# Kernel optimization log

Measured on AMD Instinct MI355X. Metric: run time of the kernel, lower is better.

## Reference

```python
import jax, jax.numpy as jnp
import numpy as np

B, T, I, H, G = 4096, 1024, 1, 16, 48  # G = 3*H gates

def _gru_layer(inp, w_ih, w_hh, b_ih, b_hh):
    # inp: [B, T, Din] -> out: [B, T, H]. PyTorch GRU gate math.
    # Precompute all input-side gate projections once (batched GEMM).
    xg = jnp.einsum('btd,gd->tbg', inp, w_ih) + b_ih  # [T, B, 3H]

    def step(h, xg_t):
        hg = h @ w_hh.T + b_hh                         # [B, 3H]
        xr, xz, xn = jnp.split(xg_t, 3, axis=-1)
        hr, hz, hn = jnp.split(hg, 3, axis=-1)
        r = jax.nn.sigmoid(xr + hr)
        z = jax.nn.sigmoid(xz + hz)
        n = jnp.tanh(xn + r * hn)
        h_new = (1.0 - z) * n + z * h
        return h_new, h_new

    h0 = jnp.zeros((inp.shape[0], H), dtype=inp.dtype)
    _, ys = jax.lax.scan(step, h0, xg)                 # ys: [T, B, H]
    return jnp.transpose(ys, (1, 0, 2))                # [B, T, H]

def setup_inputs() -> dict:
    key = jax.random.key(0)
    ks = jax.random.split(key, 8)
    s = 1.0 / np.sqrt(H)  # PyTorch default uniform(-1/sqrt(H), 1/sqrt(H))
    u = lambda k, shape: jax.random.uniform(k, shape, jnp.float32, -s, s)
    return {
        'x':      jax.random.normal(ks[0], (B, T, I), jnp.float32),
        'w_ih0':  u(ks[1], (G, I)),
        'w_ih12': u(ks[2], (2, G, H)),
        'w_hh':   u(ks[3], (3, G, H)),
        'b_ih':   u(ks[4], (3, G)),
        'b_hh':   u(ks[5], (3, G)),
        'fc_w':   u(ks[6], (5, H)),
        'fc_b':   u(ks[7], (5,)),
    }

def reference(x, w_ih0, w_ih12, w_hh, b_ih, b_hh, fc_w, fc_b):
    # 3-layer GRU (dropout=0.3 between layers is identity in eval mode)
    h = _gru_layer(x, w_ih0,     w_hh[0], b_ih[0], b_hh[0])
    h = _gru_layer(h, w_ih12[0], w_hh[1], b_ih[1], b_hh[1])
    h = _gru_layer(h, w_ih12[1], w_hh[2], b_ih[2], b_hh[2])
    # Linear head on the last timestep
    return h[:, -1, :] @ fc_w.T + fc_b                 # [B, 5]
```

## Files before the change

kernel.cpp:

```cpp
#include <hip/hip_runtime.h>
#include <stdint.h>

#define TSTEPS 1024
#define L2E 1.4426950408889634f
#define XPITCH 1028

typedef float v2f __attribute__((ext_vector_type(2)));
typedef float v4f __attribute__((ext_vector_type(4)));

__device__ __forceinline__ float rcpf_(float v) { return __builtin_amdgcn_rcpf(v); }
__device__ __forceinline__ float ex2(float v) { return __builtin_amdgcn_exp2f(v); }
#define PKFMA(a, b, c) __builtin_elementwise_fma((a), (b), (c))

__device__ __forceinline__ v2f ldg2(const float* p) {
    v2f r; uint64_t a = (uint64_t)p;
    asm volatile("global_load_dwordx2 %0, %1, off\n\ts_waitcnt vmcnt(0)"
                 : "=v"(r) : "v"(a));
    return r;
}
__device__ __forceinline__ float ldg1(const float* p) {
    float r; uint64_t a = (uint64_t)p;
    asm volatile("global_load_dword %0, %1, off\n\ts_waitcnt vmcnt(0)"
                 : "=v"(r) : "v"(a));
    return r;
}

#define RDH(dst, p)                                                        \
    do {                                                                   \
        v4f a0 = *(const v4f*)(p);                                         \
        v4f a1 = *(const v4f*)((p) + 4);                                   \
        v4f a2 = *(const v4f*)((p) + 8);                                   \
        v4f a3 = *(const v4f*)((p) + 12);                                  \
        dst[0] = __builtin_shufflevector(a0, a0, 0, 1);                    \
        dst[1] = __builtin_shufflevector(a0, a0, 2, 3);                    \
        dst[2] = __builtin_shufflevector(a1, a1, 0, 1);                    \
        dst[3] = __builtin_shufflevector(a1, a1, 2, 3);                    \
        dst[4] = __builtin_shufflevector(a2, a2, 0, 1);                    \
        dst[5] = __builtin_shufflevector(a2, a2, 2, 3);                    \
        dst[6] = __builtin_shufflevector(a3, a3, 0, 1);                    \
        dst[7] = __builtin_shufflevector(a3, a3, 2, 3);                    \
    } while (0)

#define DOT8(w, h, seed)                                                   \
    ({                                                                     \
        v2f _a = PKFMA(w[0], h[0], (seed));                                \
        _a = PKFMA(w[1], h[1], _a); _a = PKFMA(w[2], h[2], _a);            \
        _a = PKFMA(w[3], h[3], _a); _a = PKFMA(w[4], h[4], _a);            \
        _a = PKFMA(w[5], h[5], _a); _a = PKFMA(w[6], h[6], _a);            \
        _a = PKFMA(w[7], h[7], _a);                                        \
        _a.x + _a.y;                                                       \
    })
#define DOT16(wa, ha, wb, hb, seed)                                        \
    ({                                                                     \
        v2f _a = PKFMA(wa[0], ha[0], (seed));                              \
        _a = PKFMA(wa[1], ha[1], _a); _a = PKFMA(wa[2], ha[2], _a);        \
        _a = PKFMA(wa[3], ha[3], _a); _a = PKFMA(wa[4], ha[4], _a);        \
        _a = PKFMA(wa[5], ha[5], _a); _a = PKFMA(wa[6], ha[6], _a);        \
        _a = PKFMA(wa[7], ha[7], _a);                                      \
        _a = PKFMA(wb[0], hb[0], _a); _a = PKFMA(wb[1], hb[1], _a);        \
        _a = PKFMA(wb[2], hb[2], _a); _a = PKFMA(wb[3], hb[3], _a);        \
        _a = PKFMA(wb[4], hb[4], _a); _a = PKFMA(wb[5], hb[5], _a);        \
        _a = PKFMA(wb[6], hb[6], _a); _a = PKFMA(wb[7], hb[7], _a);        \
        _a.x + _a.y;                                                       \
    })

__global__ __launch_bounds__(768, 3)
__attribute__((amdgpu_waves_per_eu(3, 3)))
void gru3_ws(
    const float* __restrict__ x,
    const float* __restrict__ w_ih0,
    const float* __restrict__ w_ih12,
    const float* __restrict__ w_hh,
    const float* __restrict__ b_ih,
    const float* __restrict__ b_hh,
    const float* __restrict__ fc_w,
    const float* __restrict__ fc_b,
    float* __restrict__ out)
{
    __shared__ float xs[16 * XPITCH];
    __shared__ float hbuf[2][16][3][16];

    const int tid = threadIdx.x;
    const int wave = tid >> 6;
    const int role = wave >> 2;
    const int lane = tid & 63;
    const int s = lane >> 4;
    const int u = lane & 15;
    const int lseq = (wave & 3) * 4 + s;
    const int seq = blockIdx.x * 16 + lseq;

    {
        const float4* xg = (const float4*)(x + (size_t)blockIdx.x * 16 * TSTEPS);
#pragma unroll
        for (int j = 0; j < 6; ++j) {
            int idx = tid + 768 * j;
            if (idx < 4096) {
                float4 v = xg[idx];
                *(float4*)&xs[(idx >> 8) * XPITCH + (idx & 255) * 4] = v;
            }
        }
        ((float*)hbuf)[tid] = 0.f;
        if (tid < 1536 - 768) ((float*)hbuf)[768 + tid] = 0.f;
    }
    __syncthreads();

    if (role == 0) {
        v2f wr[8], wz[8], wn[8];
#pragma unroll
        for (int m = 0; m < 8; ++m) {
            wr[m] = ldg2(w_hh + (0 * 48 + u) * 16 + 2 * m) * -L2E;
            wz[m] = ldg2(w_hh + (0 * 48 + 16 + u) * 16 + 2 * m) * -L2E;
            wn[m] = ldg2(w_hh + (0 * 48 + 32 + u) * 16 + 2 * m) * (2.f * L2E);
        }
        const float wxr = ldg1(w_ih0 + u) * -L2E;
        const float wxz = ldg1(w_ih0 + 16 + u) * -L2E;
        const float wxn = ldg1(w_ih0 + 32 + u) * (2.f * L2E);
        const v2f sbr = {-(ldg1(b_ih + u) + ldg1(b_hh + u)) * L2E, 0.f};
        const v2f sbz = {-(ldg1(b_ih + 16 + u) + ldg1(b_hh + 16 + u)) * L2E, 0.f};
        const v2f sbn = {ldg1(b_hh + 32 + u) * (2.f * L2E), 0.f};
        const float bnx = ldg1(b_ih + 32 + u) * (2.f * L2E);
        const float* xrow = &xs[lseq * XPITCH];
        float* wb0 = &hbuf[0][lseq][0][0];
        float* wb1 = &hbuf[1][lseq][0][0];
        float hown = 0.f;
#pragma unroll 2
        for (int k = 0; k < 1026; ++k) {
            if (k < 1024) {
                const float* rb = (k & 1) ? wb0 : wb1;
                v2f hp[8];
                RDH(hp, rb);
                float xt = xrow[k];
                float sr = fmaf(wxr, xt, DOT8(wr, hp, sbr));
                float sz = fmaf(wxz, xt, DOT8(wz, hp, sbz));
                float snh = DOT8(wn, hp, sbn);
                float r = rcpf_(1.f + ex2(sr));
                float z = rcpf_(1.f + ex2(sz));
                float ut = fmaf(r, snh, fmaf(wxn, xt, bnx));
                float n = fmaf(-2.f, rcpf_(ex2(ut) + 1.f), 1.f);
                hown = fmaf(z, hown - n, n);
                ((k & 1) ? wb1 : wb0)[u] = hown;
            }
            __syncthreads();
        }
    } else if (role == 1) {
        v2f wr[8], wz[8], wn[8], vr[8], vz[8], vn[8];
#pragma unroll
        for (int m = 0; m < 8; ++m) {
            wr[m] = ldg2(w_hh + (48 + u) * 16 + 2 * m) * -L2E;
            wz[m] = ldg2(w_hh + (48 + 16 + u) * 16 + 2 * m) * -L2E;
            wn[m] = ldg2(w_hh + (48 + 32 + u) * 16 + 2 * m) * (2.f * L2E);
            vr[m] = ldg2(w_ih12 + (u) * 16 + 2 * m) * -L2E;
            vz[m] = ldg2(w_ih12 + (16 + u) * 16 + 2 * m) * -L2E;
            vn[m] = ldg2(w_ih12 + (32 + u) * 16 + 2 * m) * (2.f * L2E);
        }
        const v2f sbr = {-(ldg1(b_ih + 48 + u) + ldg1(b_hh + 48 + u)) * L2E, 0.f};
        const v2f sbz = {-(ldg1(b_ih + 64 + u) + ldg1(b_hh + 64 + u)) * L2E, 0.f};
        const v2f sbn = {ldg1(b_hh + 80 + u) * (2.f * L2E), 0.f};
        const v2f sbx = {ldg1(b_ih + 80 + u) * (2.f * L2E), 0.f};
        float* base0 = &hbuf[0][lseq][0][0];
        float* base1 = &hbuf[1][lseq][0][0];
        float hown = 0.f;
#pragma unroll 2
        for (int k = 0; k < 1026; ++k) {
            if (k >= 1 && k <= 1024) {
                const float* rb = (k & 1) ? base0 : base1;
                v2f hin[8], hp[8];
                RDH(hin, rb);
                RDH(hp, rb + 16);
                float sr = DOT16(wr, hp, vr, hin, sbr);
                float sz = DOT16(wz, hp, vz, hin, sbz);
                float snh = DOT8(wn, hp, sbn);
                float snx = DOT8(vn, hin, sbx);
                float r = rcpf_(1.f + ex2(sr));
                float z = rcpf_(1.f + ex2(sz));
                float ut = fmaf(r, snh, snx);
                float n = fmaf(-2.f, rcpf_(ex2(ut) + 1.f), 1.f);
                hown = fmaf(z, hown - n, n);
                ((k & 1) ? base1 : base0)[16 + u] = hown;
            }
            __syncthreads();
        }
    } else {
        v2f wr[8], wz[8], wn[8], vr[8], vz[8], vn[8];
#pragma unroll
        for (int m = 0; m < 8; ++m) {
            wr[m] = ldg2(w_hh + (96 + u) * 16 + 2 * m) * -L2E;
            wz[m] = ldg2(w_hh + (96 + 16 + u) * 16 + 2 * m) * -L2E;
            wn[m] = ldg2(w_hh + (96 + 32 + u) * 16 + 2 * m) * (2.f * L2E);
            vr[m] = ldg2(w_ih12 + (48 + u) * 16 + 2 * m) * -L2E;
            vz[m] = ldg2(w_ih12 + (48 + 16 + u) * 16 + 2 * m) * -L2E;
            vn[m] = ldg2(w_ih12 + (48 + 32 + u) * 16 + 2 * m) * (2.f * L2E);
        }
        const v2f sbr = {-(ldg1(b_ih + 96 + u) + ldg1(b_hh + 96 + u)) * L2E, 0.f};
        const v2f sbz = {-(ldg1(b_ih + 112 + u) + ldg1(b_hh + 112 + u)) * L2E, 0.f};
        const v2f sbn = {ldg1(b_hh + 128 + u) * (2.f * L2E), 0.f};
        const v2f sbx = {ldg1(b_ih + 128 + u) * (2.f * L2E), 0.f};
        float* base0 = &hbuf[0][lseq][0][0];
        float* base1 = &hbuf[1][lseq][0][0];
        float hown = 0.f;
#pragma unroll 2
        for (int k = 0; k < 1026; ++k) {
            if (k >= 2) {
                const float* rb = (k & 1) ? base0 : base1;
                v2f hin[8], hp[8];
                RDH(hin, rb + 16);
                RDH(hp, rb + 32);
                float sr = DOT16(wr, hp, vr, hin, sbr);
                float sz = DOT16(wz, hp, vz, hin, sbz);
                float snh = DOT8(wn, hp, sbn);
                float snx = DOT8(vn, hin, sbx);
                float r = rcpf_(1.f + ex2(sr));
                float z = rcpf_(1.f + ex2(sz));
                float ut = fmaf(r, snh, snx);
                float n = fmaf(-2.f, rcpf_(ex2(ut) + 1.f), 1.f);
                hown = fmaf(z, hown - n, n);
                ((k & 1) ? base1 : base0)[32 + u] = hown;
            }
            __syncthreads();
        }
        if (u < 5) {
            const float* h2f = &hbuf[1][lseq][2][0];
            float acc = fc_b[u];
#pragma unroll
            for (int j = 0; j < 16; ++j)
                acc = fmaf(fc_w[u * 16 + j], h2f[j], acc);
            out[seq * 5 + u] = acc;
        }
    }
}

extern "C" void kernel_launch(void* const* d_in, const int* in_sizes, int n_in,
                              void* d_out, int out_size, void* d_ws, size_t ws_size,
                              hipStream_t stream) {
    const float* x      = (const float*)d_in[0];
    const float* w_ih0  = (const float*)d_in[1];
    const float* w_ih12 = (const float*)d_in[2];
    const float* w_hh   = (const float*)d_in[3];
    const float* b_ih   = (const float*)d_in[4];
    const float* b_hh   = (const float*)d_in[5];
    const float* fc_w   = (const float*)d_in[6];
    const float* fc_b   = (const float*)d_in[7];
    float* out = (float*)d_out;

    gru3_ws<<<256, 768, 0, stream>>>(
        x, w_ih0, w_ih12, w_hh, b_ih, b_hh, fc_w, fc_b, out);
}
```

Before: 513.2 us.

## Batch four timesteps per barrier with per-layer ring buffers and smaller blocks

Measured after the change: 492.3 us. 4.1% less time.

```diff
diff --git a/kernel.cpp b/kernel.cpp
--- a/kernel.cpp
+++ b/kernel.cpp
@@ -2,6 +2,8 @@
 #include <stdint.h>
 
 #define TSTEPS 1024
+#define S 4
+#define NK 258
 #define L2E 1.4426950408889634f
 #define XPITCH 1028
 
@@ -64,9 +66,9 @@
         _a.x + _a.y;                                                       \
     })
 
-__global__ __launch_bounds__(768, 3)
+__global__ __launch_bounds__(192, 3)
 __attribute__((amdgpu_waves_per_eu(3, 3)))
-void gru3_ws(
+void gru3_sk(
     const float* __restrict__ x,
     const float* __restrict__ w_ih0,
     const float* __restrict__ w_ih12,
@@ -77,30 +79,30 @@
     const float* __restrict__ fc_b,
     float* __restrict__ out)
 {
-    __shared__ float xs[16 * XPITCH];
-    __shared__ float hbuf[2][16][3][16];
+    __shared__ float xs[4][XPITCH];
+    __shared__ float hring[3][2][S][4][16];
+    __shared__ float h2f[4][16];
 
     const int tid = threadIdx.x;
-    const int wave = tid >> 6;
-    const int role = wave >> 2;
+    const int role = tid >> 6;
     const int lane = tid & 63;
     const int s = lane >> 4;
     const int u = lane & 15;
-    const int lseq = (wave & 3) * 4 + s;
-    const int seq = blockIdx.x * 16 + lseq;
+    const int seq = blockIdx.x * 4 + s;
 
     {
-        const float4* xg = (const float4*)(x + (size_t)blockIdx.x * 16 * TSTEPS);
+        const float4* xg = (const float4*)(x + (size_t)blockIdx.x * 4 * TSTEPS);
 #pragma unroll
         for (int j = 0; j < 6; ++j) {
-            int idx = tid + 768 * j;
-            if (idx < 4096) {
+            int idx = tid + 192 * j;
+            if (idx < 1024) {
                 float4 v = xg[idx];
-                *(float4*)&xs[(idx >> 8) * XPITCH + (idx & 255) * 4] = v;
-            }
-        }
-        ((float*)hbuf)[tid] = 0.f;
-        if (tid < 1536 - 768) ((float*)hbuf)[768 + tid] = 0.f;
+                *(float4*)&xs[idx >> 8][(idx & 255) * 4] = v;
+            }
+        }
+#pragma unroll
+        for (int j = 0; j < 8; ++j)
+            ((float*)hring)[tid + 192 * j] = 0.f;
     }
     __syncthreads();
 
@@ -108,9 +110,9 @@
         v2f wr[8], wz[8], wn[8];
 #pragma unroll
         for (int m = 0; m < 8; ++m) {
-            wr[m] = ldg2(w_hh + (0 * 48 + u) * 16 + 2 * m) * -L2E;
-            wz[m] = ldg2(w_hh + (0 * 48 + 16 + u) * 16 + 2 * m) * -L2E;
-            wn[m] = ldg2(w_hh + (0 * 48 + 32 + u) * 16 + 2 * m) * (2.f * L2E);
+            wr[m] = ldg2(w_hh + (u) * 16 + 2 * m) * -L2E;
+            wz[m] = ldg2(w_hh + (16 + u) * 16 + 2 * m) * -L2E;
+            wn[m] = ldg2(w_hh + (32 + u) * 16 + 2 * m) * (2.f * L2E);
         }
         const float wxr = ldg1(w_ih0 + u) * -L2E;
         const float wxz = ldg1(w_ih0 + 16 + u) * -L2E;
@@ -119,28 +121,32 @@
         const v2f sbz = {-(ldg1(b_ih + 16 + u) + ldg1(b_hh + 16 + u)) * L2E, 0.f};
         const v2f sbn = {ldg1(b_hh + 32 + u) * (2.f * L2E), 0.f};
         const float bnx = ldg1(b_ih + 32 + u) * (2.f * L2E);
-        const float* xrow = &xs[lseq * XPITCH];
-        float* wb0 = &hbuf[0][lseq][0][0];
-        float* wb1 = &hbuf[1][lseq][0][0];
+        float* cur = &hring[0][0][0][s][0];
+        float* prv = &hring[0][1][0][s][0];
         float hown = 0.f;
-#pragma unroll 2
-        for (int k = 0; k < 1026; ++k) {
-            if (k < 1024) {
-                const float* rb = (k & 1) ? wb0 : wb1;
-                v2f hp[8];
-                RDH(hp, rb);
-                float xt = xrow[k];
-                float sr = fmaf(wxr, xt, DOT8(wr, hp, sbr));
-                float sz = fmaf(wxz, xt, DOT8(wz, hp, sbz));
-                float snh = DOT8(wn, hp, sbn);
-                float r = rcpf_(1.f + ex2(sr));
-                float z = rcpf_(1.f + ex2(sz));
-                float ut = fmaf(r, snh, fmaf(wxn, xt, bnx));
-                float n = fmaf(-2.f, rcpf_(ex2(ut) + 1.f), 1.f);
-                hown = fmaf(z, hown - n, n);
-                ((k & 1) ? wb1 : wb0)[u] = hown;
+        for (int K = 0; K < NK; ++K) {
+            if (K < 256) {
+                v4f xq = *(const v4f*)&xs[s][K * S];
+#pragma unroll
+                for (int j = 0; j < S; ++j) {
+                    const float* rb = (j == 0) ? (prv + (S - 1) * 64)
+                                               : (cur + (j - 1) * 64);
+                    v2f hp[8];
+                    RDH(hp, rb);
+                    float xt = xq[j];
+                    float sr = fmaf(wxr, xt, DOT8(wr, hp, sbr));
+                    float sz = fmaf(wxz, xt, DOT8(wz, hp, sbz));
+                    float snh = DOT8(wn, hp, sbn);
+                    float r = rcpf_(1.f + ex2(sr));
+                    float z = rcpf_(1.f + ex2(sz));
+                    float ut = fmaf(r, snh, fmaf(wxn, xt, bnx));
+                    float n = fmaf(-2.f, rcpf_(ex2(ut) + 1.f), 1.f);
+                    hown = fmaf(z, hown - n, n);
+                    cur[j * 64 + u] = hown;
+                }
             }
             __syncthreads();
+            float* t_ = cur; cur = prv; prv = t_;
         }
     } else if (role == 1) {
         v2f wr[8], wz[8], wn[8], vr[8], vz[8], vn[8];
@@ -157,28 +163,38 @@
         const v2f sbz = {-(ldg1(b_ih + 64 + u) + ldg1(b_hh + 64 + u)) * L2E, 0.f};
         const v2f sbn = {ldg1(b_hh + 80 + u) * (2.f * L2E), 0.f};
         const v2f sbx = {ldg1(b_ih + 80 + u) * (2.f * L2E), 0.f};
-        float* base0 = &hbuf[0][lseq][0][0];
-        float* base1 = &hbuf[1][lseq][0][0];
+        float* in0 = &hring[0][0][0][s][0];
+        float* in1 = &hring[0][1][0][s][0];
+        float* my0 = &hring[1][0][0][s][0];
+        float* my1 = &hring[1][1][0][s][0];
+        float* inp = in1;
+        float* mycur = my0; float* myprv = my1;
         float hown = 0.f;
-#pragma unroll 2
-        for (int k = 0; k < 1026; ++k) {
-            if (k >= 1 && k <= 1024) {
-                const float* rb = (k & 1) ? base0 : base1;
-                v2f hin[8], hp[8];
-                RDH(hin, rb);
-                RDH(hp, rb + 16);
-                float sr = DOT16(wr, hp, vr, hin, sbr);
-                float sz = DOT16(wz, hp, vz, hin, sbz);
-                float snh = DOT8(wn, hp, sbn);
-                float snx = DOT8(vn, hin, sbx);
-                float r = rcpf_(1.f + ex2(sr));
-                float z = rcpf_(1.f + ex2(sz));
-                float ut = fmaf(r, snh, snx);
-                float n = fmaf(-2.f, rcpf_(ex2(ut) + 1.f), 1.f);
-                hown = fmaf(z, hown - n, n);
-                ((k & 1) ? base1 : base0)[16 + u] = hown;
+        for (int K = 0; K < NK; ++K) {
+            if (K >= 1 && K < 257) {
+#pragma unroll
+                for (int j = 0; j < S; ++j) {
+                    const float* rin = inp + j * 64;
+                    const float* rown = (j == 0) ? (myprv + (S - 1) * 64)
+                                                 : (mycur + (j - 1) * 64);
+                    v2f hin[8], hp[8];
+                    RDH(hin, rin);
+                    RDH(hp, rown);
+                    float sr = DOT16(wr, hp, vr, hin, sbr);
+                    float sz = DOT16(wz, hp, vz, hin, sbz);
+                    float snh = DOT8(wn, hp, sbn);
+                    float snx = DOT8(vn, hin, sbx);
+                    float r = rcpf_(1.f + ex2(sr));
+                    float z = rcpf_(1.f + ex2(sz));
+                    float ut = fmaf(r, snh, snx);
+                    float n = fmaf(-2.f, rcpf_(ex2(ut) + 1.f), 1.f);
+                    hown = fmaf(z, hown - n, n);
+                    mycur[j * 64 + u] = hown;
+                }
             }
             __syncthreads();
+            float* t_ = inp == in0 ? in1 : in0; inp = t_;
+            t_ = mycur; mycur = myprv; myprv = t_;
         }
     } else {
         v2f wr[8], wz[8], wn[8], vr[8], vz[8], vn[8];
@@ -195,35 +211,45 @@
         const v2f sbz = {-(ldg1(b_ih + 112 + u) + ldg1(b_hh + 112 + u)) * L2E, 0.f};
         const v2f sbn = {ldg1(b_hh + 128 + u) * (2.f * L2E), 0.f};
         const v2f sbx = {ldg1(b_ih + 128 + u) * (2.f * L2E), 0.f};
-        float* base0 = &hbuf[0][lseq][0][0];
-        float* base1 = &hbuf[1][lseq][0][0];
+        float* in0 = &hring[1][0][0][s][0];
+        float* in1 = &hring[1][1][0][s][0];
+        float* my0 = &hring[2][0][0][s][0];
+        float* my1 = &hring[2][1][0][s][0];
+        float* inp = in1;
+        float* mycur = my0; float* myprv = my1;
         float hown = 0.f;
-#pragma unroll 2
-        for (int k = 0; k < 1026; ++k) {
-            if (k >= 2) {
-                const float* rb = (k & 1) ? base0 : base1;
-                v2f hin[8], hp[8];
-                RDH(hin, rb + 16);
-                RDH(hp, rb + 32);
-                float sr = DOT16(wr, hp, vr, hin, sbr);
-                float sz = DOT16(wz, hp, vz, hin, sbz);
-                float snh = DOT8(wn, hp, sbn);
-                float snx = DOT8(vn, hin, sbx);
-                float r = rcpf_(1.f + ex2(sr));
-                float z = rcpf_(1.f + ex2(sz));
-                float ut = fmaf(r, snh, snx);
-                float n = fmaf(-2.f, rcpf_(ex2(ut) + 1.f), 1.f);
-                hown = fmaf(z, hown - n, n);
-                ((k & 1) ? base1 : base0)[32 + u] = hown;
+        for (int K = 0; K < NK; ++K) {
+            if (K >= 2) {
+#pragma unroll
+                for (int j = 0; j < S; ++j) {
+                    const float* rin = inp + j * 64;
+                    const float* rown = (j == 0) ? (myprv + (S - 1) * 64)
+                                                 : (mycur + (j - 1) * 64);
+                    v2f hin[8], hp[8];
+                    RDH(hin, rin);
+                    RDH(hp, rown);
+                    float sr = DOT16(wr, hp, vr, hin, sbr);
+                    float sz = DOT16(wz, hp, vz, hin, sbz);
+                    float snh = DOT8(wn, hp, sbn);
+                    float snx = DOT8(vn, hin, sbx);
+                    float r = rcpf_(1.f + ex2(sr));
+                    float z = rcpf_(1.f + ex2(sz));
+                    float ut = fmaf(r, snh, snx);
+                    float n = fmaf(-2.f, rcpf_(ex2(ut) + 1.f), 1.f);
+                    hown = fmaf(z, hown - n, n);
+                    mycur[j * 64 + u] = hown;
+                }
             }
             __syncthreads();
-        }
+            float* t_ = inp == in0 ? in1 : in0; inp = t_;
+            t_ = mycur; mycur = myprv; myprv = t_;
+        }
+        h2f[s][u] = hown;
         if (u < 5) {
-            const float* h2f = &hbuf[1][lseq][2][0];
             float acc = fc_b[u];
 #pragma unroll
             for (int j = 0; j < 16; ++j)
-                acc = fmaf(fc_w[u * 16 + j], h2f[j], acc);
+                acc = fmaf(fc_w[u * 16 + j], h2f[s][j], acc);
             out[seq * 5 + u] = acc;
         }
     }
@@ -242,6 +268,6 @@
     const float* fc_b   = (const float*)d_in[7];
     float* out = (float*)d_out;
 
-    gru3_ws<<<256, 768, 0, stream>>>(
+    gru3_sk<<<1024, 192, 0, stream>>>(
         x, w_ih0, w_ih12, w_hh, b_ih, b_hh, fc_w, fc_b, out);
 }
```
